# Kernel tuning notes

Hardware: AMD Instinct MI355X
Metric: run time of the kernel (lower is better)

Reference implementation:

```python
import jax, jax.numpy as jnp
import numpy as np

H = 128  # h_size


def setup_inputs() -> dict:
    key = jax.random.key(0)
    ks = jax.random.split(key, 6)
    depth, n_trees = 16, 4
    N = 2 ** depth - 1          # nodes per complete binary tree
    T = n_trees * N             # total nodes
    return {
        "iou": jax.random.normal(ks[0], (T, 3 * H), dtype=jnp.float32),
        "h": jax.random.normal(ks[1], (T, H), dtype=jnp.float32),
        "c": jax.random.normal(ks[2], (T, H), dtype=jnp.float32),
        "W_iou": jax.random.normal(ks[3], (3 * H, 2 * H), dtype=jnp.float32) * 0.05,
        "b_iou": jnp.zeros((3 * H,), dtype=jnp.float32),
        "W_f": jax.random.normal(ks[4], (2 * H, 2 * H), dtype=jnp.float32) * 0.05,
        "b_f": jnp.zeros((2 * H,), dtype=jnp.float32),
        "depth": depth,
        "n_trees": n_trees,
    }


def _gates(iou, b_iou):
    i, o, u = jnp.split(iou + b_iou, 3, axis=1)
    return jax.nn.sigmoid(i), jax.nn.sigmoid(o), jnp.tanh(u)


def reference(iou, h, c, W_iou, b_iou, W_f, b_f, depth, n_trees):
    N = 2 ** depth - 1
    offs = (jnp.arange(n_trees) * N)[:, None]  # per-tree node offsets

    # --- leaf frontier: no messages -> apply_node_func only (keeps initial iou, c) ---
    l = depth - 1
    idx = (offs + jnp.arange(2 ** l - 1, 2 ** (l + 1) - 1)[None, :]).reshape(-1)
    i, o, u = _gates(iou[idx], b_iou)
    c_new = i * u + c[idx]
    h = h.at[idx].set(o * jnp.tanh(c_new))
    c = c.at[idx].set(c_new)

    # --- internal levels, bottom-up (level-parallel topological propagation) ---
    for l in range(depth - 2, -1, -1):
        loc = jnp.arange(2 ** l - 1, 2 ** (l + 1) - 1)
        idx = (offs + loc[None, :]).reshape(-1)
        lidx = (offs + (2 * loc + 1)[None, :]).reshape(-1)  # left child
        ridx = lidx + 1                                      # right child
        # reduce_func: gather children, forget gates, sum-reduce c, new iou
        h_cat = jnp.concatenate([h[lidx], h[ridx]], axis=-1)          # [n, 2H]
        f = jax.nn.sigmoid(h_cat @ W_f.T + b_f).reshape(-1, 2, H)     # [n, 2, H]
        c_kids = jnp.stack([c[lidx], c[ridx]], axis=1)                # [n, 2, H]
        c_red = jnp.sum(f * c_kids, axis=1)                           # [n, H]
        iou_red = h_cat @ W_iou.T                                     # [n, 3H]
        # apply_node_func
        i, o, u = _gates(iou_red, b_iou)
        c_new = i * u + c_red
        h = h.at[idx].set(o * jnp.tanh(c_new))
        c = c.at[idx].set(c_new)
    return h
```

## Files before the change

kernel.cpp:

```cpp
#include <hip/hip_runtime.h>

#define HH   128
#define H2   256
#define H3   384
#define NPT  65535
#define MT   32
#define TPB  512

typedef __bf16    bf16x8 __attribute__((ext_vector_type(8)));
typedef float     f32x4  __attribute__((ext_vector_type(4)));
typedef _Float16  f16x4  __attribute__((ext_vector_type(4)));
typedef _Float16  half_t;

typedef __attribute__((address_space(1))) const unsigned int gref_u32;
typedef __attribute__((address_space(3))) unsigned int       lref_u32;

__device__ unsigned short Wb_g[640 * 256];

__device__ __forceinline__ float fsig(float x)  { return 1.0f / (1.0f + __expf(-x)); }
__device__ __forceinline__ float ftanh(float x) { return 1.0f - 2.0f / (__expf(2.0f * x) + 1.0f); }
__device__ __forceinline__ unsigned short f2bf(float f) {
    unsigned u = __float_as_uint(f);
    u += 0x7fffu + ((u >> 16) & 1u);
    return (unsigned short)(u >> 16);
}
__device__ __forceinline__ int swz(int off) { return off ^ (((off >> 9) & 7) << 4); }

__global__ __launch_bounds__(256) void conv_k(const float* __restrict__ W_iou,
                                              const float* __restrict__ W_f)
{
    int t    = blockIdx.x * 256 + threadIdx.x;
    int base = t * 4;
    int j = base >> 8, k = base & 255;
    const float* src = (j < H3) ? (W_iou + j * H2 + k)
                                : (W_f + (j - H3) * H2 + k);
    float4 v = *(const float4*)src;
    ushort4 p;
    p.x = f2bf(v.x); p.y = f2bf(v.y); p.z = f2bf(v.z); p.w = f2bf(v.w);
    *(ushort4*)(Wb_g + base) = p;
}

__global__ __launch_bounds__(256) void leaf_k(
    const float* __restrict__ iou, const float* __restrict__ c_in,
    const float* __restrict__ b_iou,
    float* __restrict__ h_out, half_t* __restrict__ c_ws,
    unsigned short* __restrict__ h_bf)
{
    int g    = blockIdx.x * 256 + threadIdx.x;
    int node = g >> 5;
    int e    = (g & 31) << 2;
    int tree = node >> 15;
    int loc  = 32767 + (node & 32767);
    int row  = tree * NPT + loc;

    const float* ip = iou + (size_t)row * H3;
    float4 vi = *(const float4*)(ip + e);
    float4 vo = *(const float4*)(ip + HH + e);
    float4 vu = *(const float4*)(ip + 2 * HH + e);
    float4 vc = *(const float4*)(c_in + row * HH + e);
    float4 bi = *(const float4*)(b_iou + e);
    float4 bo = *(const float4*)(b_iou + HH + e);
    float4 bu = *(const float4*)(b_iou + 2 * HH + e);

    float4 hn, cn;
#define DOL(X) { float iv = fsig(vi.X + bi.X); float ov = fsig(vo.X + bo.X); \
                 float uv = ftanh(vu.X + bu.X); float cv = iv * uv + vc.X;   \
                 cn.X = cv; hn.X = ov * ftanh(cv); }
    DOL(x) DOL(y) DOL(z) DOL(w)
#undef DOL
    *(float4*)(h_out + row * HH + e) = hn;
    f16x4 cf; cf.x = (half_t)cn.x; cf.y = (half_t)cn.y; cf.z = (half_t)cn.z; cf.w = (half_t)cn.w;
    *(f16x4*)(c_ws + row * HH + e) = cf;
    ushort4 hb;
    hb.x = f2bf(hn.x); hb.y = f2bf(hn.y); hb.z = f2bf(hn.z); hb.w = f2bf(hn.w);
    *(ushort4*)(h_bf + row * HH + e) = hb;
}

__device__ __forceinline__ void mfma_from(const unsigned char* tile,
                                          const unsigned short* Wp,
                                          f32x4 acc[2][5], int lr, int lc)
{
#pragma unroll
    for (int kk = 0; kk < 8; ++kk) {
        bf16x8 a0 = *(const bf16x8*)(tile + swz(lr * 512 + kk * 64 + lc * 16));
        bf16x8 a1 = *(const bf16x8*)(tile + swz((16 + lr) * 512 + kk * 64 + lc * 16));
#pragma unroll
        for (int g = 0; g < 5; ++g) {
            bf16x8 b = *(const bf16x8*)(Wp + g * HH * H2 + kk * 32);
            acc[0][g] = __builtin_amdgcn_mfma_f32_16x16x32_bf16(a0, b, acc[0][g], 0, 0, 0);
            acc[1][g] = __builtin_amdgcn_mfma_f32_16x16x32_bf16(a1, b, acc[1][g], 0, 0, 0);
        }
    }
}

#define GATES(AC, MTI, RI, CL, CR, HV, CV) \
    { float pi = AC[MTI][0][RI] + bi, po = AC[MTI][1][RI] + bo, pu = AC[MTI][2][RI] + bu; \
      float pl = AC[MTI][3][RI] + bl, pr = AC[MTI][4][RI] + br;                           \
      CV = fsig(pi) * ftanh(pu) + fsig(pl) * (CL) + fsig(pr) * (CR);                      \
      HV = fsig(po) * ftanh(CV); }

__device__ __forceinline__ void do_tile(
    int lvl, int tile,
    float bi, float bo, float bu, float bl, float br,
    float* __restrict__ h_g, half_t* __restrict__ c_ws,
    unsigned short* __restrict__ h_bf,
    unsigned short* A_lds, unsigned short* C_lds,
    int tid, int w, int lr, int lc, int ee)
{
    const int node0 = tile * MT;
    const int loc0  = (1 << lvl) - 1;
    const int lmask = loc0;

    __syncthreads();

#pragma unroll
    for (int it = 0; it < 2; ++it) {
        int item = tid + TPB * it;
        int m = item >> 5, u = item & 31;
        int node = node0 + m;
        int tree = node >> lvl;
        int loc  = loc0 + (node & lmask);
        int pairE = (tree * NPT + 2 * loc + 1) * HH;
        int sb    = (u * 16) ^ ((m & 7) << 4);
        __builtin_amdgcn_global_load_lds(
            (gref_u32*)((const char*)h_bf + (size_t)pairE * 2 + sb),
            (lref_u32*)((char*)A_lds + item * 16), 16, 0, 0);
        __builtin_amdgcn_global_load_lds(
            (gref_u32*)((const char*)c_ws + (size_t)pairE * 2 + sb),
            (lref_u32*)((char*)C_lds + item * 16), 16, 0, 0);
    }
    __syncthreads();

    int rofs[2][4];
#pragma unroll
    for (int mt = 0; mt < 2; ++mt)
#pragma unroll
        for (int r = 0; r < 4; ++r) {
            int node = node0 + mt * 16 + lc * 4 + r;
            int tree = node >> lvl;
            int loc  = loc0 + (node & lmask);
            rofs[mt][r] = (tree * NPT + loc) * HH + ee;
        }

    f32x4 acc[2][5] = {};
    const unsigned short* Wp = Wb_g + ee * H2 + lc * 8;
    mfma_from((const unsigned char*)A_lds, Wp, acc, lr, lc);

#pragma unroll
    for (int mt = 0; mt < 2; ++mt)
#pragma unroll
        for (int r = 0; r < 4; ++r) {
            int m  = mt * 16 + lc * 4 + r;
            int cb = m * 512 + ((ee * 2) ^ ((m & 7) << 4));
            float cl = (float)*(const half_t*)((const char*)C_lds + cb);
            float cr = (float)*(const half_t*)((const char*)C_lds + cb + 256);
            float hv, cv;
            GATES(acc, mt, r, cl, cr, hv, cv);
            int o = rofs[mt][r];
            h_g[o]  = hv;
            c_ws[o] = (half_t)cv;
            h_bf[o] = f2bf(hv);
        }
}

__global__ __launch_bounds__(TPB, 4) void level_k(
    int lvl,
    const float* __restrict__ b_iou, const float* __restrict__ b_f,
    float* __restrict__ h_g, half_t* __restrict__ c_ws,
    unsigned short* __restrict__ h_bf)
{
    __shared__ __align__(16) unsigned short A_lds[MT * H2];
    __shared__ __align__(16) unsigned short C_lds[MT * H2];
    const int tid = threadIdx.x;
    const int w = tid >> 6, lr = tid & 15, lc = (tid & 63) >> 4;
    const int ee = w * 16 + lr;
    const float bi = b_iou[ee], bo = b_iou[HH + ee], bu = b_iou[2 * HH + ee];
    const float bl = b_f[ee],   br = b_f[HH + ee];
    do_tile(lvl, blockIdx.x, bi, bo, bu, bl, br, h_g, c_ws, h_bf,
            A_lds, C_lds, tid, w, lr, lc, ee);
}

__global__ __launch_bounds__(TPB, 2) void solo_k(
    const float* __restrict__ b_iou, const float* __restrict__ b_f,
    float* __restrict__ h_g, half_t* __restrict__ c_ws,
    const unsigned short* __restrict__ h_bf)
{
    __shared__ __align__(16) unsigned char hb[32768];

    const int tid = threadIdx.x;
    const int w = tid >> 6, lr = tid & 15, lc = (tid & 63) >> 4;
    const int ee = w * 16 + lr;
    const int tb = blockIdx.x * NPT;
    const float bi = b_iou[ee], bo = b_iou[HH + ee], bu = b_iou[2 * HH + ee];
    const float bl = b_f[ee],   br = b_f[HH + ee];

    bf16x8 Bf[5][8];
    const unsigned short* Wp = Wb_g + ee * H2 + lc * 8;
#pragma unroll
    for (int g = 0; g < 5; ++g)
#pragma unroll
        for (int kk = 0; kk < 8; ++kk)
            Bf[g][kk] = *(const bf16x8*)(Wp + g * HH * H2 + kk * 32);

#pragma unroll
    for (int it = 0; it < 2; ++it) {
        int p = tid + TPB * it;
        int cc = p >> 4, q = p & 15;
        uint4 v = *(const uint4*)(h_bf + (tb + 63 + cc) * HH + q * 8);
        *(uint4*)(hb + swz(p * 16)) = v;
    }

#pragma unroll 1
    for (int l = 5; l >= 0; --l) {
        const int nl     = 1 << l;
        const int loc0   = nl - 1;
        const int cloc0  = 2 * nl - 1;
        const int cbase  = (l & 1) ? 0 : 16384;
        const int obase  = cbase ^ 16384;
        const bool mt1   = (nl > 16);

        __syncthreads();

        f32x4 acc[2][5] = {};
#pragma unroll
        for (int kk = 0; kk < 8; ++kk) {
            bf16x8 a0 = *(const bf16x8*)(hb + cbase + swz(lr * 512 + kk * 64 + lc * 16));
#pragma unroll
            for (int g = 0; g < 5; ++g)
                acc[0][g] = __builtin_amdgcn_mfma_f32_16x16x32_bf16(a0, Bf[g][kk], acc[0][g], 0, 0, 0);
            if (mt1) {
                bf16x8 a1 = *(const bf16x8*)(hb + cbase + swz((16 + lr) * 512 + kk * 64 + lc * 16));
#pragma unroll
                for (int g = 0; g < 5; ++g)
                    acc[1][g] = __builtin_amdgcn_mfma_f32_16x16x32_bf16(a1, Bf[g][kk], acc[1][g], 0, 0, 0);
            }
        }
        __syncthreads();

#pragma unroll
        for (int mt = 0; mt < 2; ++mt)
#pragma unroll
            for (int r = 0; r < 4; ++r) {
                int j = mt * 16 + lc * 4 + r;
                if (j >= nl) continue;
                int row  = tb + loc0 + j;
                int lrow = tb + cloc0 + 2 * j;
                float hv, cv;
                GATES(acc, mt, r, (float)c_ws[lrow * HH + ee], (float)c_ws[lrow * HH + HH + ee], hv, cv);
                h_g[row * HH + ee]  = hv;
                c_ws[row * HH + ee] = (half_t)cv;
                *(unsigned short*)(hb + obase + swz(j * 256 + ee * 2)) = f2bf(hv);
            }
    }
}

extern "C" void kernel_launch(void* const* d_in, const int* in_sizes, int n_in,
                              void* d_out, int out_size, void* d_ws, size_t ws_size,
                              hipStream_t stream)
{
    const float* iou   = (const float*)d_in[0];
    const float* c_in  = (const float*)d_in[2];
    const float* W_iou = (const float*)d_in[3];
    const float* b_iou = (const float*)d_in[4];
    const float* W_f   = (const float*)d_in[5];
    const float* b_f   = (const float*)d_in[6];
    float* h_out = (float*)d_out;
    half_t* c_ws = (half_t*)d_ws;
    unsigned short* h_bf = (unsigned short*)((char*)d_ws + (size_t)72 * 1024 * 1024);

    conv_k<<<160, 256, 0, stream>>>(W_iou, W_f);
    leaf_k<<<16384, 256, 0, stream>>>(iou, c_in, b_iou, h_out, c_ws, h_bf);

    for (int l = 14; l >= 6; --l) {
        int blocks = (4 << l) / MT;
        level_k<<<blocks, TPB, 0, stream>>>(l, b_iou, b_f, h_out, c_ws, h_bf);
    }
    solo_k<<<4, TPB, 0, stream>>>(b_iou, b_f, h_out, c_ws, h_bf);
}
```

Before: 367.9 us.

## Shrink level kernel tile to 16 nodes with 256 threads and direct c loads

The level kernel now handles 16 nodes per block with 256 threads, where each wave computes 32 output columns (two B fragments) against a single A fragment, instead of 32 nodes with 512 threads. The child cell states are no longer staged through LDS. They are read straight from global memory in the gate epilogue. This doubles the block count, halves LDS use per block and raises the occupancy target, aiming for better latency hiding and less LDS traffic. In exchange, each block reads the weights for fewer nodes, so weight reuse per load drops, and the scattered half-precision c loads come from global memory.

```diff
diff --git a/kernel.cpp b/kernel.cpp
--- a/kernel.cpp
+++ b/kernel.cpp
@@ -4,7 +4,6 @@
 #define H2   256
 #define H3   384
 #define NPT  65535
-#define MT   32
 #define TPB  512
 
 typedef __bf16    bf16x8 __attribute__((ext_vector_type(8)));
@@ -76,46 +75,25 @@
     *(ushort4*)(h_bf + row * HH + e) = hb;
 }
 
-__device__ __forceinline__ void mfma_from(const unsigned char* tile,
-                                          const unsigned short* Wp,
-                                          f32x4 acc[2][5], int lr, int lc)
-{
-#pragma unroll
-    for (int kk = 0; kk < 8; ++kk) {
-        bf16x8 a0 = *(const bf16x8*)(tile + swz(lr * 512 + kk * 64 + lc * 16));
-        bf16x8 a1 = *(const bf16x8*)(tile + swz((16 + lr) * 512 + kk * 64 + lc * 16));
-#pragma unroll
-        for (int g = 0; g < 5; ++g) {
-            bf16x8 b = *(const bf16x8*)(Wp + g * HH * H2 + kk * 32);
-            acc[0][g] = __builtin_amdgcn_mfma_f32_16x16x32_bf16(a0, b, acc[0][g], 0, 0, 0);
-            acc[1][g] = __builtin_amdgcn_mfma_f32_16x16x32_bf16(a1, b, acc[1][g], 0, 0, 0);
-        }
-    }
-}
-
-#define GATES(AC, MTI, RI, CL, CR, HV, CV) \
-    { float pi = AC[MTI][0][RI] + bi, po = AC[MTI][1][RI] + bo, pu = AC[MTI][2][RI] + bu; \
-      float pl = AC[MTI][3][RI] + bl, pr = AC[MTI][4][RI] + br;                           \
-      CV = fsig(pi) * ftanh(pu) + fsig(pl) * (CL) + fsig(pr) * (CR);                      \
-      HV = fsig(po) * ftanh(CV); }
-
-__device__ __forceinline__ void do_tile(
-    int lvl, int tile,
-    float bi, float bo, float bu, float bl, float br,
+__global__ __launch_bounds__(256, 8) void level_k(
+    int lvl,
+    const float* __restrict__ b_iou, const float* __restrict__ b_f,
     float* __restrict__ h_g, half_t* __restrict__ c_ws,
-    unsigned short* __restrict__ h_bf,
-    unsigned short* A_lds, unsigned short* C_lds,
-    int tid, int w, int lr, int lc, int ee)
-{
-    const int node0 = tile * MT;
+    unsigned short* __restrict__ h_bf)
+{
+    __shared__ __align__(16) unsigned short A_lds[16 * H2];
+
+    const int tid = threadIdx.x;
+    const int w  = tid >> 6;
+    const int lr = tid & 15;
+    const int lc = (tid & 63) >> 4;
+    const int node0 = blockIdx.x * 16;
     const int loc0  = (1 << lvl) - 1;
     const int lmask = loc0;
 
-    __syncthreads();
-
 #pragma unroll
     for (int it = 0; it < 2; ++it) {
-        int item = tid + TPB * it;
+        int item = tid + 256 * it;
         int m = item >> 5, u = item & 31;
         int node = node0 + m;
         int tree = node >> lvl;
@@ -125,59 +103,51 @@
         __builtin_amdgcn_global_load_lds(
             (gref_u32*)((const char*)h_bf + (size_t)pairE * 2 + sb),
             (lref_u32*)((char*)A_lds + item * 16), 16, 0, 0);
-        __builtin_amdgcn_global_load_lds(
-            (gref_u32*)((const char*)c_ws + (size_t)pairE * 2 + sb),
-            (lref_u32*)((char*)C_lds + item * 16), 16, 0, 0);
     }
     __syncthreads();
 
-    int rofs[2][4];
-#pragma unroll
-    for (int mt = 0; mt < 2; ++mt)
+    f32x4 acc[2][5] = {};
+    const unsigned short* Wp0 = Wb_g + (w * 32 + lr) * H2 + lc * 8;
+    const unsigned short* Wp1 = Wp0 + 16 * H2;
+#pragma unroll
+    for (int kk = 0; kk < 8; ++kk) {
+        bf16x8 a0 = *(const bf16x8*)((const char*)A_lds + swz(lr * 512 + kk * 64 + lc * 16));
+#pragma unroll
+        for (int g = 0; g < 5; ++g) {
+            bf16x8 b0 = *(const bf16x8*)(Wp0 + g * HH * H2 + kk * 32);
+            bf16x8 b1 = *(const bf16x8*)(Wp1 + g * HH * H2 + kk * 32);
+            acc[0][g] = __builtin_amdgcn_mfma_f32_16x16x32_bf16(a0, b0, acc[0][g], 0, 0, 0);
+            acc[1][g] = __builtin_amdgcn_mfma_f32_16x16x32_bf16(a0, b1, acc[1][g], 0, 0, 0);
+        }
+    }
+
+#pragma unroll
+    for (int sub = 0; sub < 2; ++sub) {
+        const int ee = w * 32 + sub * 16 + lr;
+        const float bi = b_iou[ee], bo = b_iou[HH + ee], bu = b_iou[2 * HH + ee];
+        const float bl = b_f[ee],   br = b_f[HH + ee];
 #pragma unroll
         for (int r = 0; r < 4; ++r) {
-            int node = node0 + mt * 16 + lc * 4 + r;
+            int node = node0 + lc * 4 + r;
             int tree = node >> lvl;
             int loc  = loc0 + (node & lmask);
-            rofs[mt][r] = (tree * NPT + loc) * HH + ee;
-        }
-
-    f32x4 acc[2][5] = {};
-    const unsigned short* Wp = Wb_g + ee * H2 + lc * 8;
-    mfma_from((const unsigned char*)A_lds, Wp, acc, lr, lc);
-
-#pragma unroll
-    for (int mt = 0; mt < 2; ++mt)
-#pragma unroll
-        for (int r = 0; r < 4; ++r) {
-            int m  = mt * 16 + lc * 4 + r;
-            int cb = m * 512 + ((ee * 2) ^ ((m & 7) << 4));
-            float cl = (float)*(const half_t*)((const char*)C_lds + cb);
-            float cr = (float)*(const half_t*)((const char*)C_lds + cb + 256);
-            float hv, cv;
-            GATES(acc, mt, r, cl, cr, hv, cv);
-            int o = rofs[mt][r];
+            int base = tree * NPT + loc;
+            int o    = base * HH + ee;
+            int lro  = (base + loc + 1) * HH + ee;
+            float cl = (float)c_ws[lro];
+            float cr = (float)c_ws[lro + HH];
+            float pi = acc[sub][0][r] + bi;
+            float po = acc[sub][1][r] + bo;
+            float pu = acc[sub][2][r] + bu;
+            float pl = acc[sub][3][r] + bl;
+            float pr = acc[sub][4][r] + br;
+            float cv = fsig(pi) * ftanh(pu) + fsig(pl) * cl + fsig(pr) * cr;
+            float hv = fsig(po) * ftanh(cv);
             h_g[o]  = hv;
             c_ws[o] = (half_t)cv;
             h_bf[o] = f2bf(hv);
         }
-}
-
-__global__ __launch_bounds__(TPB, 4) void level_k(
-    int lvl,
-    const float* __restrict__ b_iou, const float* __restrict__ b_f,
-    float* __restrict__ h_g, half_t* __restrict__ c_ws,
-    unsigned short* __restrict__ h_bf)
-{
-    __shared__ __align__(16) unsigned short A_lds[MT * H2];
-    __shared__ __align__(16) unsigned short C_lds[MT * H2];
-    const int tid = threadIdx.x;
-    const int w = tid >> 6, lr = tid & 15, lc = (tid & 63) >> 4;
-    const int ee = w * 16 + lr;
-    const float bi = b_iou[ee], bo = b_iou[HH + ee], bu = b_iou[2 * HH + ee];
-    const float bl = b_f[ee],   br = b_f[HH + ee];
-    do_tile(lvl, blockIdx.x, bi, bo, bu, bl, br, h_g, c_ws, h_bf,
-            A_lds, C_lds, tid, w, lr, lc, ee);
+    }
 }
 
 __global__ __launch_bounds__(TPB, 2) void solo_k(
@@ -245,8 +215,15 @@
                 if (j >= nl) continue;
                 int row  = tb + loc0 + j;
                 int lrow = tb + cloc0 + 2 * j;
-                float hv, cv;
-                GATES(acc, mt, r, (float)c_ws[lrow * HH + ee], (float)c_ws[lrow * HH + HH + ee], hv, cv);
+                float cl = (float)c_ws[lrow * HH + ee];
+                float cr = (float)c_ws[lrow * HH + HH + ee];
+                float pi = acc[mt][0][r] + bi;
+                float po = acc[mt][1][r] + bo;
+                float pu = acc[mt][2][r] + bu;
+                float pl = acc[mt][3][r] + bl;
+                float pr = acc[mt][4][r] + br;
+                float cv = fsig(pi) * ftanh(pu) + fsig(pl) * cl + fsig(pr) * cr;
+                float hv = fsig(po) * ftanh(cv);
                 h_g[row * HH + ee]  = hv;
                 c_ws[row * HH + ee] = (half_t)cv;
                 *(unsigned short*)(hb + obase + swz(j * 256 + ee * 2)) = f2bf(hv);
@@ -272,8 +249,8 @@
     leaf_k<<<16384, 256, 0, stream>>>(iou, c_in, b_iou, h_out, c_ws, h_bf);
 
     for (int l = 14; l >= 6; --l) {
-        int blocks = (4 << l) / MT;
-        level_k<<<blocks, TPB, 0, stream>>>(l, b_iou, b_f, h_out, c_ws, h_bf);
+        int blocks = (4 << l) / 16;
+        level_k<<<blocks, 256, 0, stream>>>(l, b_iou, b_f, h_out, c_ws, h_bf);
     }
     solo_k<<<4, TPB, 0, stream>>>(b_iou, b_f, h_out, c_ws, h_bf);
 }
```

Measured after the change: 842.7 us. 129% more time.
